# Kernel optimization log

Hardware: AMD Instinct MI355X
Metric: run time of the kernel (lower is better)

Reference implementation:

```python
import jax, jax.numpy as jnp
import numpy as np

B, N, D, H = 2, 2048, 2048, 16
HD = D // H  # head_dim = 128
EPS = 1e-06

def rmsnorm(x, w, eps=EPS):
    xf = x.astype(jnp.float32)
    y = xf * jax.lax.rsqrt(jnp.mean(xf * xf, axis=-1, keepdims=True) + eps)
    return y.astype(x.dtype) * w

def rope_apply(x, freqs, num_heads):
    # x: [B, S, D]; freqs: [S, 1, HD//2, 2] = (cos, sin) of complex rotation
    b, s, d = x.shape
    hd = d // num_heads
    xr = x.reshape(b, s, num_heads, hd // 2, 2)
    x0, x1 = xr[..., 0], xr[..., 1]
    fr, fi = freqs[..., 0], freqs[..., 1]  # broadcast [S,1,HD//2] over heads
    out = jnp.stack([x0 * fr - x1 * fi, x0 * fi + x1 * fr], axis=-1)
    return out.reshape(b, s, d).astype(x.dtype)

def attention(q, k, v, num_heads):
    b, s, d = q.shape
    hd = d // num_heads
    qh = q.reshape(b, s, num_heads, hd).transpose(0, 2, 1, 3)  # b h s d
    kh = k.reshape(b, s, num_heads, hd).transpose(0, 2, 1, 3)
    vh = v.reshape(b, s, num_heads, hd).transpose(0, 2, 1, 3)
    scale = hd ** -0.5
    scores = jnp.einsum('bhqd,bhkd->bhqk', qh, kh) * scale
    probs = jax.nn.softmax(scores, axis=-1)
    out = jnp.einsum('bhqk,bhkd->bhqd', probs, vh)
    return out.transpose(0, 2, 1, 3).reshape(b, s, d)

def setup_inputs() -> dict:
    key = jax.random.key(0)
    ks = jax.random.split(key, 8)
    x = jax.random.normal(ks[0], (B, N, D), jnp.float32)
    # standard RoPE frequencies
    pos = jnp.arange(N, dtype=jnp.float32)
    inv = 1.0 / (10000.0 ** (jnp.arange(0, HD, 2, dtype=jnp.float32) / HD))
    ang = pos[:, None] * inv[None, :]  # [N, HD//2]
    freqs = jnp.stack([jnp.cos(ang), jnp.sin(ang)], axis=-1)[:, None, :, :]  # [N,1,HD//2,2]
    s = 0.02
    wq = jax.random.normal(ks[1], (D, D), jnp.float32) * s
    wk = jax.random.normal(ks[2], (D, D), jnp.float32) * s
    wv = jax.random.normal(ks[3], (D, D), jnp.float32) * s
    wo = jax.random.normal(ks[4], (D, D), jnp.float32) * s
    bq = jnp.zeros((D,), jnp.float32)
    bk = jnp.zeros((D,), jnp.float32)
    bv = jnp.zeros((D,), jnp.float32)
    bo = jnp.zeros((D,), jnp.float32)
    gq = jnp.ones((D,), jnp.float32)
    gk = jnp.ones((D,), jnp.float32)
    return {"x": x, "freqs": freqs, "wq": wq, "bq": bq, "wk": wk, "bk": bk,
            "wv": wv, "bv": bv, "wo": wo, "bo": bo, "gq": gq, "gk": gk}

def reference(x, freqs, wq, bq, wk, bk, wv, bv, wo, bo, gq, gk):
    q = rmsnorm(x @ wq.T + bq, gq)
    k = rmsnorm(x @ wk.T + bk, gk)
    v = x @ wv.T + bv
    q = rope_apply(q, freqs, H)
    k = rope_apply(k, freqs, H)
    attn_out = attention(q, k, v, H)
    return attn_out @ wo.T + bo
```

## Files before the change

kernel.cpp:

```cpp
#include <hip/hip_runtime.h>
#include <hip/hip_bf16.h>
#include <stdint.h>


typedef __bf16 bf16;
typedef __bf16 bf16x8 __attribute__((ext_vector_type(8)));
typedef __bf16 bf16x4 __attribute__((ext_vector_type(4)));
typedef float  f32x4  __attribute__((ext_vector_type(4)));

#define MTOT   4096
#define DMODEL 2048
#define NSEQ   2048
#define NHEAD  16
#define HDIM   128

static __device__ __forceinline__ void async_ld16(const void* g, void* l) {
  void* gnc = const_cast<void*>(g);
  __builtin_amdgcn_global_load_lds((__attribute__((address_space(1))) void*)gnc,
                                   (__attribute__((address_space(3))) void*)l,
                                   16, 0, 0);
}

#define XG (MTOT * DMODEL / 8)
#define WG (DMODEL * DMODEL / 8)

__global__ __launch_bounds__(256) void k_cvt4(
    const float* __restrict__ x, const float* __restrict__ wq,
    const float* __restrict__ wk, const float* __restrict__ wv,
    bf16* __restrict__ xb, bf16* __restrict__ wqb, bf16* __restrict__ wkb,
    bf16* __restrict__ wvb) {
  int stride = gridDim.x * blockDim.x;
  for (int i = blockIdx.x * blockDim.x + threadIdx.x; i < XG + 3 * WG;
       i += stride) {
    const float* src;
    bf16* dst;
    int off;
    if (i < XG) { src = x; dst = xb; off = i; }
    else if (i < XG + WG) { src = wq; dst = wqb; off = i - XG; }
    else if (i < XG + 2 * WG) { src = wk; dst = wkb; off = i - XG - WG; }
    else { src = wv; dst = wvb; off = i - XG - 2 * WG; }
    const float4* p = (const float4*)(src) + 2 * (size_t)off;
    float4 a = p[0], b = p[1];
    bf16x8 o;
    o[0] = (bf16)a.x; o[1] = (bf16)a.y; o[2] = (bf16)a.z; o[3] = (bf16)a.w;
    o[4] = (bf16)b.x; o[5] = (bf16)b.y; o[6] = (bf16)b.z; o[7] = (bf16)b.w;
    *((bf16x8*)(dst) + off) = o;
  }
}

__global__ __launch_bounds__(256) void k_cvt(const float* __restrict__ in,
                                             bf16* __restrict__ out, int n8) {
  int stride = gridDim.x * blockDim.x;
  for (int i = blockIdx.x * blockDim.x + threadIdx.x; i < n8; i += stride) {
    const float4* p = (const float4*)(in) + 2 * (size_t)i;
    float4 a = p[0], b = p[1];
    bf16x8 o;
    o[0] = (bf16)a.x; o[1] = (bf16)a.y; o[2] = (bf16)a.z; o[3] = (bf16)a.w;
    o[4] = (bf16)b.x; o[5] = (bf16)b.y; o[6] = (bf16)b.z; o[7] = (bf16)b.w;
    *((bf16x8*)(out) + i) = o;
  }
}

#define BUFELEMS (384 * 64)

template <int OUTMODE>
static __device__ __forceinline__ void gemm256_body(
    const bf16* __restrict__ A, const bf16* __restrict__ W,
    const float* __restrict__ bias, void* __restrict__ outp, int m0, int n0) {
  extern __shared__ __align__(16) bf16 dynls[];

  const int tid = threadIdx.x;
  const int lane = tid & 63, w = tid >> 6;
  const int wm = w >> 2, wn = w & 3;
  const int g = lane >> 4, r0 = lane & 15;

  f32x4 acc[4][4];
  const f32x4 vzero = {0.f, 0.f, 0.f, 0.f};
#pragma unroll
  for (int i = 0; i < 4; ++i)
#pragma unroll
    for (int j = 0; j < 4; ++j) acc[i][j] = vzero;

  const bf16* Abase = A + (size_t)m0 * DMODEL;
  const bf16* Wbase = W + (size_t)n0 * DMODEL;

  auto stage_a = [&](int kt, int buf) {
    const bf16* asrc = Abase + kt * 64;
    const bf16* bsrc = Wbase + kt * 64;
    bf16* sBuf = dynls + buf * BUFELEMS;
#pragma unroll
    for (int p = 0; p < 2; ++p) {
      int ch = tid + p * 512;
      int row = ch >> 3, c = (ch & 7) ^ (row & 7);
      async_ld16(asrc + (size_t)row * DMODEL + c * 8, sBuf + ch * 8);
    }
    {
      int ch = tid;
      int row = ch >> 3, c = (ch & 7) ^ (row & 7);
      async_ld16(bsrc + (size_t)row * DMODEL + c * 8, sBuf + 128 * 64 + ch * 8);
    }
  };
  auto stage_b = [&](int kt, int buf) {
    const bf16* bsrc = Wbase + kt * 64;
    bf16* sBuf = dynls + buf * BUFELEMS + 128 * 64;
#pragma unroll
    for (int p = 1; p < 4; ++p) {
      int ch = tid + p * 512;
      int row = ch >> 3, c = (ch & 7) ^ (row & 7);
      async_ld16(bsrc + (size_t)row * DMODEL + c * 8, sBuf + ch * 8);
    }
  };

  const int NT = DMODEL / 64;
  stage_a(0, 0); stage_b(0, 0);
  stage_a(1, 1); stage_b(1, 1);
  asm volatile("s_waitcnt vmcnt(6)" ::: "memory");
  __builtin_amdgcn_s_barrier();

  for (int kt = 0; kt < NT; ++kt) {
    const bf16* sA = dynls + (kt % 3) * BUFELEMS;
    const bf16* sB = sA + 128 * 64;
    const bool pf = (kt + 2) < NT;
    const int nb = (kt + 2) % 3;

#pragma unroll
    for (int ks = 0; ks < 2; ++ks) {
      bf16x8 af[4], bfr[4];
      const int cc = ks * 4 + g;
#pragma unroll
      for (int i = 0; i < 4; ++i) {
        int ra = wm * 64 + i * 16 + r0;
        af[i] = *(const bf16x8*)(sA + ra * 64 + ((cc ^ (ra & 7)) << 3));
        int rb = wn * 64 + i * 16 + r0;
        bfr[i] = *(const bf16x8*)(sB + rb * 64 + ((cc ^ (rb & 7)) << 3));
      }
      if (ks == 0) {
        if (pf) stage_a(kt + 2, nb);
      } else {
        if (pf) {
          stage_b(kt + 2, nb);
          asm volatile("s_waitcnt vmcnt(6)" ::: "memory");
        } else {
          asm volatile("s_waitcnt vmcnt(0)" ::: "memory");
        }
      }
      __builtin_amdgcn_sched_barrier(0);
      __builtin_amdgcn_s_barrier();
      __builtin_amdgcn_sched_barrier(0);
      __builtin_amdgcn_s_setprio(1);
#pragma unroll
      for (int i = 0; i < 4; ++i)
#pragma unroll
        for (int j = 0; j < 4; ++j)
          acc[i][j] = __builtin_amdgcn_mfma_f32_16x16x32_bf16(af[i], bfr[j],
                                                              acc[i][j], 0, 0, 0);
      __builtin_amdgcn_s_setprio(0);
    }
  }

#pragma unroll
  for (int i = 0; i < 4; ++i) {
#pragma unroll
    for (int j = 0; j < 4; ++j) {
      int mb = m0 + wm * 64 + i * 16 + g * 4;
      int n = n0 + wn * 64 + j * 16 + r0;
      float bn = bias[n];
      if (OUTMODE == 0) {
        bf16* o = (bf16*)outp;
#pragma unroll
        for (int r = 0; r < 4; ++r)
          o[(size_t)(mb + r) * DMODEL + n] = (bf16)(acc[i][j][r] + bn);
      } else if (OUTMODE == 2) {
        float* o = (float*)outp;
#pragma unroll
        for (int r = 0; r < 4; ++r)
          o[(size_t)(mb + r) * DMODEL + n] = acc[i][j][r] + bn;
      } else {
        bf16* o = (bf16*)outp;
        int bb = mb >> 11, s = mb & (NSEQ - 1);
        bf16x4 pk;
#pragma unroll
        for (int r = 0; r < 4; ++r) pk[r] = (bf16)(acc[i][j][r] + bn);
        *(bf16x4*)(o + (size_t)(bb * DMODEL + n) * NSEQ + s) = pk;
      }
    }
  }
}

__global__ __launch_bounds__(512, 2) void k_gemm_qkv(
    const bf16* __restrict__ xb, const bf16* __restrict__ wq,
    const bf16* __restrict__ wk, const bf16* __restrict__ wv,
    const float* __restrict__ bq, const float* __restrict__ bk,
    const float* __restrict__ bv, bf16* __restrict__ q, bf16* __restrict__ k,
    bf16* __restrict__ vt) {
  int nb = blockIdx.x;
  int m0 = blockIdx.y * 128;
  int sec = nb >> 3;
  int n0 = (nb & 7) * 256;
  if (sec == 0)
    gemm256_body<0>(xb, wq, bq, q, m0, n0);
  else if (sec == 1)
    gemm256_body<0>(xb, wk, bk, k, m0, n0);
  else
    gemm256_body<1>(xb, wv, bv, vt, m0, n0);
}

__global__ __launch_bounds__(512, 2) void k_gemm_out(
    const bf16* __restrict__ ab, const bf16* __restrict__ wo,
    const float* __restrict__ bo, float* __restrict__ out) {
  gemm256_body<2>(ab, wo, bo, out, blockIdx.y * 128, blockIdx.x * 256);
}

__global__ __launch_bounds__(256) void k_norm_rope(
    bf16* __restrict__ q, bf16* __restrict__ kk, const float* __restrict__ gq,
    const float* __restrict__ gk, const float* __restrict__ freqs) {
  int bidx = blockIdx.x;
  bf16* buf = (bidx < MTOT) ? q : kk;
  const float* gw = (bidx < MTOT) ? gq : gk;
  float qs = (bidx < MTOT) ? 0.08838834764831845f : 1.0f;
  int row = bidx & (MTOT - 1);
  int s = row & (NSEQ - 1);
  int tid = threadIdx.x;
  int i0 = tid * 8;
  bf16* ptr = buf + (size_t)row * DMODEL + i0;
  bf16x8 v = *(const bf16x8*)ptr;
  float x[8];
  float ssq = 0.f;
#pragma unroll
  for (int j = 0; j < 8; ++j) {
    x[j] = (float)v[j];
    ssq += x[j] * x[j];
  }
#pragma unroll
  for (int off = 1; off < 64; off <<= 1) ssq += __shfl_xor(ssq, off);
  __shared__ float part[4];
  if ((tid & 63) == 0) part[tid >> 6] = ssq;
  __syncthreads();
  float tot = part[0] + part[1] + part[2] + part[3];
  float sc = rsqrtf(tot * (1.f / DMODEL) + 1e-6f) * qs;
  float4 g0 = *(const float4*)(gw + i0);
  float4 g1 = *(const float4*)(gw + i0 + 4);
  float y[8];
  y[0] = x[0] * sc * g0.x; y[1] = x[1] * sc * g0.y;
  y[2] = x[2] * sc * g0.z; y[3] = x[3] * sc * g0.w;
  y[4] = x[4] * sc * g1.x; y[5] = x[5] * sc * g1.y;
  y[6] = x[6] * sc * g1.z; y[7] = x[7] * sc * g1.w;
  int dl = i0 & (HDIM - 1);
  const float* fp = freqs + (size_t)s * HDIM + dl;
  float4 f0 = *(const float4*)fp;
  float4 f1 = *(const float4*)(fp + 4);
  bf16x8 out;
  out[0] = (bf16)(y[0] * f0.x - y[1] * f0.y);
  out[1] = (bf16)(y[0] * f0.y + y[1] * f0.x);
  out[2] = (bf16)(y[2] * f0.z - y[3] * f0.w);
  out[3] = (bf16)(y[2] * f0.w + y[3] * f0.z);
  out[4] = (bf16)(y[4] * f1.x - y[5] * f1.y);
  out[5] = (bf16)(y[4] * f1.y + y[5] * f1.x);
  out[6] = (bf16)(y[6] * f1.z - y[7] * f1.w);
  out[7] = (bf16)(y[6] * f1.w + y[7] * f1.z);
  *(bf16x8*)ptr = out;
}

__global__ __launch_bounds__(512, 4) void k_attn(const bf16* __restrict__ q,
                                                 const bf16* __restrict__ k,
                                                 const bf16* __restrict__ vt,
                                                 bf16* __restrict__ o) {
  __shared__ __align__(16) bf16 sk[2][64 * 128];
  __shared__ __align__(16) bf16 sv[2][128 * 64];
  const int bid = blockIdx.x;
  const int idx = bid >> 3;
  const int bh = (bid & 7) * 4 + (idx >> 4);
  const int qt = idx & 15;
  const int bb = bh >> 4, h = bh & 15;
  const int tid = threadIdx.x;
  const int lane = tid & 63, w = tid >> 6;
  const int g = lane >> 4, r0 = lane & 15;

  bf16x8 qf[4];
  {
    const bf16* qbase =
        q + (size_t)(bb * NSEQ + qt * 128 + w * 16 + r0) * DMODEL + h * HDIM;
#pragma unroll
    for (int ds = 0; ds < 4; ++ds)
      qf[ds] = *(const bf16x8*)(qbase + ds * 32 + g * 8);
  }
  f32x4 oacc[8];
  const f32x4 vzero = {0.f, 0.f, 0.f, 0.f};
#pragma unroll
  for (int dt = 0; dt < 8; ++dt) oacc[dt] = vzero;
  float m = -3.0e38f, l = 0.f;

  const bf16* kbase = k + (size_t)(bb * NSEQ) * DMODEL + h * HDIM;
  const bf16* vbase = vt + (size_t)(bb * DMODEL + h * HDIM) * NSEQ;

  const int s0lane = ((lane & 16) << 1) | r0;
  const int s1lane = s0lane | 16;
  const bool hi5 = (lane & 32) != 0;

  auto stage = [&](int t, int buf) {
    int k0 = t * 64;
#pragma unroll
    for (int p = 0; p < 2; ++p) {
      int ch = tid + p * 512;
      int row = ch >> 4, cs = ch & 15;
      int c = cs ^ (row & 7);
      async_ld16(kbase + (size_t)(k0 + row) * DMODEL + c * 8, &sk[buf][ch * 8]);
    }
#pragma unroll
    for (int p = 0; p < 2; ++p) {
      int ch = tid + p * 512;
      int row = ch >> 3, cs = ch & 7;
      int c = cs ^ (row & 7);
      async_ld16(vbase + (size_t)row * NSEQ + k0 + c * 8, &sv[buf][ch * 8]);
    }
  };

  stage(0, 0);
  for (int t = 0; t < NSEQ / 64; ++t) {
    const int cur = t & 1;
    asm volatile("s_waitcnt vmcnt(0)" ::: "memory");
    __syncthreads();
    if (t + 1 < NSEQ / 64) stage(t + 1, cur ^ 1);

    f32x4 sacc[4];
#pragma unroll
    for (int kkt = 0; kkt < 4; ++kkt) sacc[kkt] = vzero;
#pragma unroll
    for (int kkt = 0; kkt < 4; ++kkt) {
      int rk = kkt * 16 + r0;
#pragma unroll
      for (int ds = 0; ds < 4; ++ds) {
        int c = ds * 4 + g;
        bf16x8 kf = *(const bf16x8*)(&sk[cur][rk * 128 + ((c ^ (rk & 7)) << 3)]);
        sacc[kkt] =
            __builtin_amdgcn_mfma_f32_16x16x32_bf16(kf, qf[ds], sacc[kkt], 0, 0, 0);
      }
    }

    float pm = sacc[0][0];
#pragma unroll
    for (int kkt = 0; kkt < 4; ++kkt)
#pragma unroll
      for (int r = 0; r < 4; ++r) pm = fmaxf(pm, sacc[kkt][r]);
    pm = fmaxf(pm, __shfl_xor(pm, 16));
    pm = fmaxf(pm, __shfl_xor(pm, 32));
    const int need = __any(pm > m);
    const float mu = need ? fmaxf(m, pm) : m;

    uint32_t W[4][2];
    float rs = 0.f;
#pragma unroll
    for (int kkt = 0; kkt < 4; ++kkt) {
      float p0 = __expf(sacc[kkt][0] - mu);
      float p1 = __expf(sacc[kkt][1] - mu);
      float p2 = __expf(sacc[kkt][2] - mu);
      float p3 = __expf(sacc[kkt][3] - mu);
      rs += (p0 + p1) + (p2 + p3);
      asm("v_cvt_pk_bf16_f32 %0, %1, %2" : "=v"(W[kkt][0]) : "v"(p0), "v"(p1));
      asm("v_cvt_pk_bf16_f32 %0, %1, %2" : "=v"(W[kkt][1]) : "v"(p2), "v"(p3));
    }
    rs += __shfl_xor(rs, 16);
    rs += __shfl_xor(rs, 32);

    if (need) {
      float alpha = __expf(m - mu);
      m = mu;
      l = l * alpha + rs;
      float a4[4];
#pragma unroll
      for (int r = 0; r < 4; ++r)
        a4[r] = __shfl(alpha, (lane & 48) | (g * 4 + r));
#pragma unroll
      for (int dt = 0; dt < 8; ++dt)
#pragma unroll
        for (int r = 0; r < 4; ++r) oacc[dt][r] *= a4[r];
    } else {
      l += rs;
    }

#pragma unroll
    for (int ks = 0; ks < 2; ++ks) {
      union { uint32_t u[4]; bf16x8 v; } pa;
#pragma unroll
      for (int ww = 0; ww < 4; ++ww) {
        int src = (ww < 2) ? s0lane : s1lane;
        int lo = __shfl((int)W[2 * ks][ww & 1], src);
        int hv = __shfl((int)W[2 * ks + 1][ww & 1], src);
        pa.u[ww] = hi5 ? (uint32_t)hv : (uint32_t)lo;
      }
#pragma unroll
      for (int dt = 0; dt < 8; ++dt) {
        int rv = dt * 16 + r0;
        int c = ks * 4 + g;
        bf16x8 vf = *(const bf16x8*)(&sv[cur][rv * 64 + ((c ^ (rv & 7)) << 3)]);
        oacc[dt] =
            __builtin_amdgcn_mfma_f32_16x16x32_bf16(pa.v, vf, oacc[dt], 0, 0, 0);
      }
    }
  }

  float rl[4];
#pragma unroll
  for (int r = 0; r < 4; ++r) {
    float lr = __shfl(l, (lane & 48) | (g * 4 + r));
    rl[r] = 1.f / lr;
  }
  bf16* obase =
      o + (size_t)(bb * NSEQ + qt * 128 + w * 16 + g * 4) * DMODEL + h * HDIM;
#pragma unroll
  for (int dt = 0; dt < 8; ++dt)
#pragma unroll
    for (int r = 0; r < 4; ++r)
      obase[(size_t)r * DMODEL + dt * 16 + r0] = (bf16)(oacc[dt][r] * rl[r]);
}

extern "C" void kernel_launch(void* const* d_in, const int* in_sizes, int n_in,
                              void* d_out, int out_size, void* d_ws,
                              size_t ws_size, hipStream_t stream) {
  (void)in_sizes; (void)n_in; (void)out_size; (void)ws_size;
  const float* x = (const float*)d_in[0];
  const float* freqs = (const float*)d_in[1];
  const float* wq = (const float*)d_in[2];
  const float* bq = (const float*)d_in[3];
  const float* wk = (const float*)d_in[4];
  const float* bk = (const float*)d_in[5];
  const float* wv = (const float*)d_in[6];
  const float* bv = (const float*)d_in[7];
  const float* wo = (const float*)d_in[8];
  const float* bo = (const float*)d_in[9];
  const float* gq = (const float*)d_in[10];
  const float* gk = (const float*)d_in[11];

  char* ws = (char*)d_ws;
  const size_t SZ_TOK = (size_t)MTOT * DMODEL * sizeof(bf16);
  const size_t SZ_W = (size_t)DMODEL * DMODEL * sizeof(bf16);
  bf16* xb = (bf16*)ws;
  bf16* qb = (bf16*)(ws + SZ_TOK);
  bf16* kb = (bf16*)(ws + 2 * SZ_TOK);
  bf16* vtb = (bf16*)(ws + 3 * SZ_TOK);
  bf16* wqb = (bf16*)(ws + 4 * SZ_TOK);
  bf16* wkb = (bf16*)(ws + 4 * SZ_TOK + SZ_W);
  bf16* wvb = (bf16*)(ws + 4 * SZ_TOK + 2 * SZ_W);

  const int LDSB = 3 * BUFELEMS * (int)sizeof(bf16);
  hipFuncSetAttribute((const void*)k_gemm_qkv,
                      hipFuncAttributeMaxDynamicSharedMemorySize, LDSB);
  hipFuncSetAttribute((const void*)k_gemm_out,
                      hipFuncAttributeMaxDynamicSharedMemorySize, LDSB);

  k_cvt4<<<2048, 256, 0, stream>>>(x, wq, wk, wv, xb, wqb, wkb, wvb);

  k_gemm_qkv<<<dim3(24, 32), 512, LDSB, stream>>>(xb, wqb, wkb, wvb, bq, bk,
                                                  bv, qb, kb, vtb);
  k_cvt<<<1024, 256, 0, stream>>>(wo, wqb, (DMODEL * DMODEL) / 8);

  k_norm_rope<<<2 * MTOT, 256, 0, stream>>>(qb, kb, gq, gk, freqs);

  k_attn<<<512, 512, 0, stream>>>(qb, kb, vtb, xb);

  k_gemm_out<<<dim3(8, 32), 512, LDSB, stream>>>(xb, wqb, bo, (float*)d_out);
}
```

Baseline: 302.0 us.

## Rewrite attention kernel with 32x32x16 MFMA and transposed scores layout

The flash-attention kernel now uses 4 waves of 256 threads, each owning 32 query rows, and issues 32x32x16 bf16 MFMAs in place of 16x16x32. Scores are computed as K·Q^T so every lane holds one query's values. The row max and row sum then need only a permlane32_swap, not cross-lane shuffles, and the P fragment for the PV matmul is rebuilt with permlane32 swaps. It also adds a lazy rescale that only updates the running max when it grows by more than 8, which skips most rescaling work but lets exponentials exceed 1 by up to e^8. Per-wave LDS reuse rises at the cost of more registers and fewer waves per block.

```diff
diff --git a/kernel.cpp b/kernel.cpp
--- a/kernel.cpp
+++ b/kernel.cpp
@@ -7,6 +7,8 @@
 typedef __bf16 bf16x8 __attribute__((ext_vector_type(8)));
 typedef __bf16 bf16x4 __attribute__((ext_vector_type(4)));
 typedef float  f32x4  __attribute__((ext_vector_type(4)));
+typedef float  f32x16 __attribute__((ext_vector_type(16)));
+typedef unsigned int uint2v __attribute__((ext_vector_type(2)));
 
 #define MTOT   4096
 #define DMODEL 2048
@@ -261,7 +263,7 @@
   *(bf16x8*)ptr = out;
 }
 
-__global__ __launch_bounds__(512, 4) void k_attn(const bf16* __restrict__ q,
+__global__ __launch_bounds__(256, 2) void k_attn(const bf16* __restrict__ q,
                                                  const bf16* __restrict__ k,
                                                  const bf16* __restrict__ vt,
                                                  bf16* __restrict__ o) {
@@ -274,41 +276,39 @@
   const int bb = bh >> 4, h = bh & 15;
   const int tid = threadIdx.x;
   const int lane = tid & 63, w = tid >> 6;
-  const int g = lane >> 4, r0 = lane & 15;
-
-  bf16x8 qf[4];
+  const int l31 = lane & 31, b5 = lane >> 5;
+
+  bf16x8 qf[8];
   {
-    const bf16* qbase =
-        q + (size_t)(bb * NSEQ + qt * 128 + w * 16 + r0) * DMODEL + h * HDIM;
-#pragma unroll
-    for (int ds = 0; ds < 4; ++ds)
-      qf[ds] = *(const bf16x8*)(qbase + ds * 32 + g * 8);
-  }
-  f32x4 oacc[8];
-  const f32x4 vzero = {0.f, 0.f, 0.f, 0.f};
-#pragma unroll
-  for (int dt = 0; dt < 8; ++dt) oacc[dt] = vzero;
+    const bf16* qb =
+        q + (size_t)(bb * NSEQ + qt * 128 + w * 32 + l31) * DMODEL + h * HDIM +
+        b5 * 8;
+#pragma unroll
+    for (int kk = 0; kk < 8; ++kk) qf[kk] = *(const bf16x8*)(qb + kk * 16);
+  }
+
+  f32x16 oacc[4];
+#pragma unroll
+  for (int dt = 0; dt < 4; ++dt)
+#pragma unroll
+    for (int r = 0; r < 16; ++r) oacc[dt][r] = 0.f;
   float m = -3.0e38f, l = 0.f;
 
   const bf16* kbase = k + (size_t)(bb * NSEQ) * DMODEL + h * HDIM;
   const bf16* vbase = vt + (size_t)(bb * DMODEL + h * HDIM) * NSEQ;
 
-  const int s0lane = ((lane & 16) << 1) | r0;
-  const int s1lane = s0lane | 16;
-  const bool hi5 = (lane & 32) != 0;
-
   auto stage = [&](int t, int buf) {
     int k0 = t * 64;
 #pragma unroll
-    for (int p = 0; p < 2; ++p) {
-      int ch = tid + p * 512;
+    for (int p = 0; p < 4; ++p) {
+      int ch = tid + p * 256;
       int row = ch >> 4, cs = ch & 15;
       int c = cs ^ (row & 7);
       async_ld16(kbase + (size_t)(k0 + row) * DMODEL + c * 8, &sk[buf][ch * 8]);
     }
 #pragma unroll
-    for (int p = 0; p < 2; ++p) {
-      int ch = tid + p * 512;
+    for (int p = 0; p < 4; ++p) {
+      int ch = tid + p * 256;
       int row = ch >> 3, cs = ch & 7;
       int c = cs ^ (row & 7);
       async_ld16(vbase + (size_t)row * NSEQ + k0 + c * 8, &sv[buf][ch * 8]);
@@ -322,96 +322,115 @@
     __syncthreads();
     if (t + 1 < NSEQ / 64) stage(t + 1, cur ^ 1);
 
-    f32x4 sacc[4];
-#pragma unroll
-    for (int kkt = 0; kkt < 4; ++kkt) sacc[kkt] = vzero;
-#pragma unroll
-    for (int kkt = 0; kkt < 4; ++kkt) {
-      int rk = kkt * 16 + r0;
-#pragma unroll
-      for (int ds = 0; ds < 4; ++ds) {
-        int c = ds * 4 + g;
-        bf16x8 kf = *(const bf16x8*)(&sk[cur][rk * 128 + ((c ^ (rk & 7)) << 3)]);
-        sacc[kkt] =
-            __builtin_amdgcn_mfma_f32_16x16x32_bf16(kf, qf[ds], sacc[kkt], 0, 0, 0);
-      }
-    }
-
-    float pm = sacc[0][0];
-#pragma unroll
-    for (int kkt = 0; kkt < 4; ++kkt)
-#pragma unroll
-      for (int r = 0; r < 4; ++r) pm = fmaxf(pm, sacc[kkt][r]);
-    pm = fmaxf(pm, __shfl_xor(pm, 16));
-    pm = fmaxf(pm, __shfl_xor(pm, 32));
-    const int need = __any(pm > m);
-    const float mu = need ? fmaxf(m, pm) : m;
-
-    uint32_t W[4][2];
+    f32x16 sacc[2];
+#pragma unroll
+    for (int s = 0; s < 2; ++s)
+#pragma unroll
+      for (int r = 0; r < 16; ++r) sacc[s][r] = 0.f;
+#pragma unroll
+    for (int s = 0; s < 2; ++s) {
+      const int row = s * 32 + l31;
+#pragma unroll
+      for (int kk = 0; kk < 8; ++kk) {
+        const int c = 2 * kk + b5;
+        bf16x8 kf = *(const bf16x8*)(&sk[cur][row * 128 + ((c ^ (row & 7)) << 3)]);
+        sacc[s] = __builtin_amdgcn_mfma_f32_32x32x16_bf16(kf, qf[kk], sacc[s],
+                                                          0, 0, 0);
+      }
+    }
+
+    float t1[8];
+#pragma unroll
+    for (int i = 0; i < 8; ++i)
+      t1[i] = fmaxf(fmaxf(sacc[0][2 * i], sacc[0][2 * i + 1]),
+                    fmaxf(sacc[1][2 * i], sacc[1][2 * i + 1]));
+    float pm = fmaxf(fmaxf(fmaxf(t1[0], t1[1]), fmaxf(t1[2], t1[3])),
+                     fmaxf(fmaxf(t1[4], t1[5]), fmaxf(t1[6], t1[7])));
+    {
+      uint2v r2 = __builtin_amdgcn_permlane32_swap(__float_as_uint(pm),
+                                                   __float_as_uint(pm), false,
+                                                   false);
+      pm = fmaxf(__uint_as_float(r2.x), __uint_as_float(r2.y));
+    }
+    const int need = __any(pm > m + 8.0f);
+    if (need) {
+      float mn = fmaxf(m, pm);
+      float alpha = __expf(m - mn);
+      m = mn;
+      l *= alpha;
+#pragma unroll
+      for (int dt = 0; dt < 4; ++dt)
+#pragma unroll
+        for (int r = 0; r < 16; ++r) oacc[dt][r] *= alpha;
+    }
+
     float rs = 0.f;
 #pragma unroll
-    for (int kkt = 0; kkt < 4; ++kkt) {
-      float p0 = __expf(sacc[kkt][0] - mu);
-      float p1 = __expf(sacc[kkt][1] - mu);
-      float p2 = __expf(sacc[kkt][2] - mu);
-      float p3 = __expf(sacc[kkt][3] - mu);
-      rs += (p0 + p1) + (p2 + p3);
-      asm("v_cvt_pk_bf16_f32 %0, %1, %2" : "=v"(W[kkt][0]) : "v"(p0), "v"(p1));
-      asm("v_cvt_pk_bf16_f32 %0, %1, %2" : "=v"(W[kkt][1]) : "v"(p2), "v"(p3));
-    }
-    rs += __shfl_xor(rs, 16);
-    rs += __shfl_xor(rs, 32);
-
-    if (need) {
-      float alpha = __expf(m - mu);
-      m = mu;
-      l = l * alpha + rs;
-      float a4[4];
-#pragma unroll
-      for (int r = 0; r < 4; ++r)
-        a4[r] = __shfl(alpha, (lane & 48) | (g * 4 + r));
-#pragma unroll
-      for (int dt = 0; dt < 8; ++dt)
-#pragma unroll
-        for (int r = 0; r < 4; ++r) oacc[dt][r] *= a4[r];
-    } else {
-      l += rs;
-    }
-
-#pragma unroll
-    for (int ks = 0; ks < 2; ++ks) {
-      union { uint32_t u[4]; bf16x8 v; } pa;
-#pragma unroll
-      for (int ww = 0; ww < 4; ++ww) {
-        int src = (ww < 2) ? s0lane : s1lane;
-        int lo = __shfl((int)W[2 * ks][ww & 1], src);
-        int hv = __shfl((int)W[2 * ks + 1][ww & 1], src);
-        pa.u[ww] = hi5 ? (uint32_t)hv : (uint32_t)lo;
-      }
-#pragma unroll
-      for (int dt = 0; dt < 8; ++dt) {
-        int rv = dt * 16 + r0;
-        int c = ks * 4 + g;
-        bf16x8 vf = *(const bf16x8*)(&sv[cur][rv * 64 + ((c ^ (rv & 7)) << 3)]);
-        oacc[dt] =
-            __builtin_amdgcn_mfma_f32_16x16x32_bf16(pa.v, vf, oacc[dt], 0, 0, 0);
-      }
-    }
-  }
-
-  float rl[4];
-#pragma unroll
-  for (int r = 0; r < 4; ++r) {
-    float lr = __shfl(l, (lane & 48) | (g * 4 + r));
-    rl[r] = 1.f / lr;
-  }
-  bf16* obase =
-      o + (size_t)(bb * NSEQ + qt * 128 + w * 16 + g * 4) * DMODEL + h * HDIM;
-#pragma unroll
-  for (int dt = 0; dt < 8; ++dt)
-#pragma unroll
-    for (int r = 0; r < 4; ++r)
-      obase[(size_t)r * DMODEL + dt * 16 + r0] = (bf16)(oacc[dt][r] * rl[r]);
+    for (int s = 0; s < 2; ++s)
+#pragma unroll
+      for (int r = 0; r < 16; ++r) {
+        float pv = __expf(sacc[s][r] - m);
+        sacc[s][r] = pv;
+        rs += pv;
+      }
+    {
+      uint2v r2 = __builtin_amdgcn_permlane32_swap(__float_as_uint(rs),
+                                                   __float_as_uint(rs), false,
+                                                   false);
+      rs = __uint_as_float(r2.x) + __uint_as_float(r2.y);
+    }
+    l += rs;
+
+    uint32_t P2[16];
+#pragma unroll
+    for (int s = 0; s < 2; ++s)
+#pragma unroll
+      for (int i = 0; i < 8; ++i)
+        asm("v_cvt_pk_bf16_f32 %0, %1, %2"
+            : "=v"(P2[s * 8 + i])
+            : "v"(sacc[s][2 * i]), "v"(sacc[s][2 * i + 1]));
+
+#pragma unroll
+    for (int s = 0; s < 2; ++s) {
+#pragma unroll
+      for (int u = 0; u < 2; ++u) {
+        union { uint32_t uw[4]; bf16x8 v; } pb;
+        uint2v ra = __builtin_amdgcn_permlane32_swap(P2[s * 8 + 4 * u],
+                                                     P2[s * 8 + 4 * u + 2],
+                                                     false, false);
+        uint2v rb = __builtin_amdgcn_permlane32_swap(P2[s * 8 + 4 * u + 1],
+                                                     P2[s * 8 + 4 * u + 3],
+                                                     false, false);
+        pb.uw[0] = ra.x;
+        pb.uw[1] = rb.x;
+        pb.uw[2] = ra.y;
+        pb.uw[3] = rb.y;
+        const int c = 4 * s + 2 * u + b5;
+#pragma unroll
+        for (int dt = 0; dt < 4; ++dt) {
+          const int rv = dt * 32 + l31;
+          bf16x8 vf =
+              *(const bf16x8*)(&sv[cur][rv * 64 + ((c ^ (rv & 7)) << 3)]);
+          oacc[dt] = __builtin_amdgcn_mfma_f32_32x32x16_bf16(vf, pb.v, oacc[dt],
+                                                             0, 0, 0);
+        }
+      }
+    }
+  }
+
+  const float rl = 1.f / l;
+  bf16* ob = o + (size_t)(bb * NSEQ + qt * 128 + w * 32 + l31) * DMODEL +
+             h * HDIM;
+#pragma unroll
+  for (int dt = 0; dt < 4; ++dt) {
+#pragma unroll
+    for (int rg = 0; rg < 4; ++rg) {
+      bf16x4 pk4;
+#pragma unroll
+      for (int e = 0; e < 4; ++e) pk4[e] = (bf16)(oacc[dt][rg * 4 + e] * rl);
+      *(bf16x4*)(ob + dt * 32 + rg * 8 + b5 * 4) = pk4;
+    }
+  }
 }
 
 extern "C" void kernel_launch(void* const* d_in, const int* in_sizes, int n_in,
@@ -456,7 +475,7 @@
 
   k_norm_rope<<<2 * MTOT, 256, 0, stream>>>(qb, kb, gq, gk, freqs);
 
-  k_attn<<<512, 512, 0, stream>>>(qb, kb, vtb, xb);
+  k_attn<<<512, 256, 0, stream>>>(qb, kb, vtb, xb);
 
   k_gemm_out<<<dim3(8, 32), 512, LDSB, stream>>>(xb, wqb, bo, (float*)d_out);
 }
```

After: 270.2 us. 10.5% less time.
